# Optimization experiments

Measured on AMD Instinct MI355X. Metric: run time of the kernel, lower is better.

## Reference

```python
import jax, jax.numpy as jnp
import numpy as np

B, T, D = 16, 512, 512
T_OUT = 2560  # static cap on expanded length (mean total ~2048, +3 sigma << 2560)
MAX_DUR = 8.0


def setup_inputs() -> dict:
    key = jax.random.key(0)
    kx, kd = jax.random.split(key)
    x = jax.random.normal(kx, (B, T, D), dtype=jnp.float32)
    dur = jax.random.uniform(kd, (B, T), dtype=jnp.float32) * MAX_DUR
    return {"x": x, "dur": dur}


def reference(x, dur):
    # Rounded integer durations: (dur + 0.5).long() in torch == floor(dur + 0.5)
    d = jnp.floor(dur + 0.5).astype(jnp.int32)          # [B, T]
    ends = jnp.cumsum(d, axis=1)                         # [B, T] exclusive-end offsets
    pos = jnp.arange(T_OUT, dtype=jnp.int32)             # [T_OUT]
    # For output frame j, source phoneme = first t with ends[t] > j
    src = jax.vmap(lambda e: jnp.searchsorted(e, pos, side='right'))(ends)  # [B, T_OUT]
    src = jnp.minimum(src, x.shape[1] - 1)
    out = jnp.take_along_axis(x, src[:, :, None], axis=1)  # [B, T_OUT, D]
    valid = (pos[None, :] < ends[:, -1:]).astype(x.dtype)  # zero-pad beyond total length
    return out * valid[:, :, None]
```

## Files before the change

kernel.cpp:

```cpp
#include <hip/hip_runtime.h>
#include <math.h>


#define LR_B 16
#define LR_T 512
#define LR_D 512
#define LR_TOUT 2560

__global__ void lr_scan_kernel(const float* __restrict__ dur, int* __restrict__ ends) {
    const int b = blockIdx.x;
    const int t = threadIdx.x;
    __shared__ int s[LR_T];
    float dv = dur[b * LR_T + t];
    s[t] = (int)floorf(dv + 0.5f);
    __syncthreads();
    #pragma unroll
    for (int off = 1; off < LR_T; off <<= 1) {
        int v = (t >= off) ? s[t - off] : 0;
        __syncthreads();
        s[t] += v;
        __syncthreads();
    }
    ends[b * LR_T + t] = s[t];
}

__global__ void lr_expand_kernel(const float* __restrict__ x,
                                 const int* __restrict__ ends,
                                 float* __restrict__ out) {
    const int j = blockIdx.x;
    const int b = blockIdx.y;
    const int tid = threadIdx.x;

    const int* e = ends + b * LR_T;
    const int total = e[LR_T - 1];

    float4 val = make_float4(0.f, 0.f, 0.f, 0.f);
    if (j < total) {
        int lo = 0, hi = LR_T;
        while (lo < hi) {
            int mid = (lo + hi) >> 1;
            if (e[mid] > j) hi = mid; else lo = mid + 1;
        }
        int src = (lo < LR_T - 1) ? lo : (LR_T - 1);
        const float4* row = (const float4*)(x + (size_t)(b * LR_T + src) * LR_D);
        val = row[tid];
    }
    float4* orow = (float4*)(out + (size_t)(b * LR_TOUT + j) * LR_D);
    orow[tid] = val;
}

extern "C" void kernel_launch(void* const* d_in, const int* in_sizes, int n_in,
                              void* d_out, int out_size, void* d_ws, size_t ws_size,
                              hipStream_t stream) {
    const float* x   = (const float*)d_in[0];
    const float* dur = (const float*)d_in[1];
    float* out = (float*)d_out;
    int* ends = (int*)d_ws;

    lr_scan_kernel<<<LR_B, LR_T, 0, stream>>>(dur, ends);

    dim3 grid(LR_TOUT, LR_B);
    lr_expand_kernel<<<grid, 128, 0, stream>>>(x, ends, out);
}
```

Baseline: 112.4 us.

## Precompute source indices in scan kernel and process two rows per block

```diff
diff --git a/kernel.cpp b/kernel.cpp
--- a/kernel.cpp
+++ b/kernel.cpp
@@ -7,7 +7,7 @@
 #define LR_D 512
 #define LR_TOUT 2560
 
-__global__ void lr_scan_kernel(const float* __restrict__ dur, int* __restrict__ ends) {
+__global__ void lr_prep_kernel(const float* __restrict__ dur, int* __restrict__ src) {
     const int b = blockIdx.x;
     const int t = threadIdx.x;
     __shared__ int s[LR_T];
@@ -21,32 +21,43 @@
         s[t] += v;
         __syncthreads();
     }
-    ends[b * LR_T + t] = s[t];
+    const int total = s[LR_T - 1];
+    #pragma unroll
+    for (int k = 0; k < LR_TOUT / LR_T; ++k) {
+        const int j = t + k * LR_T;
+        int v;
+        if (j < total) {
+            int lo = 0, hi = LR_T;
+            #pragma unroll
+            for (int it = 0; it < 10; ++it) {
+                if (lo < hi) {
+                    int mid = (lo + hi) >> 1;
+                    if (s[mid] > j) hi = mid; else lo = mid + 1;
+                }
+            }
+            v = (lo < LR_T - 1) ? lo : (LR_T - 1);
+        } else {
+            v = -1;
+        }
+        src[b * LR_TOUT + j] = v;
+    }
 }
 
 __global__ void lr_expand_kernel(const float* __restrict__ x,
-                                 const int* __restrict__ ends,
+                                 const int* __restrict__ src,
                                  float* __restrict__ out) {
-    const int j = blockIdx.x;
     const int b = blockIdx.y;
-    const int tid = threadIdx.x;
+    const int j = blockIdx.x * 2 + (threadIdx.x >> 7);
+    const int lane = threadIdx.x & 127;
 
-    const int* e = ends + b * LR_T;
-    const int total = e[LR_T - 1];
-
+    const int si = src[b * LR_TOUT + j];
     float4 val = make_float4(0.f, 0.f, 0.f, 0.f);
-    if (j < total) {
-        int lo = 0, hi = LR_T;
-        while (lo < hi) {
-            int mid = (lo + hi) >> 1;
-            if (e[mid] > j) hi = mid; else lo = mid + 1;
-        }
-        int src = (lo < LR_T - 1) ? lo : (LR_T - 1);
-        const float4* row = (const float4*)(x + (size_t)(b * LR_T + src) * LR_D);
-        val = row[tid];
+    if (si >= 0) {
+        const float4* row = (const float4*)(x + (size_t)(b * LR_T + si) * LR_D);
+        val = row[lane];
     }
     float4* orow = (float4*)(out + (size_t)(b * LR_TOUT + j) * LR_D);
-    orow[tid] = val;
+    orow[lane] = val;
 }
 
 extern "C" void kernel_launch(void* const* d_in, const int* in_sizes, int n_in,
@@ -55,10 +66,10 @@
     const float* x   = (const float*)d_in[0];
     const float* dur = (const float*)d_in[1];
     float* out = (float*)d_out;
-    int* ends = (int*)d_ws;
+    int* src = (int*)d_ws;
 
-    lr_scan_kernel<<<LR_B, LR_T, 0, stream>>>(dur, ends);
+    lr_prep_kernel<<<LR_B, LR_T, 0, stream>>>(dur, src);
 
-    dim3 grid(LR_TOUT, LR_B);
-    lr_expand_kernel<<<grid, 128, 0, stream>>>(x, ends, out);
+    dim3 grid(LR_TOUT / 2, LR_B);
+    lr_expand_kernel<<<grid, 256, 0, stream>>>(x, src, out);
 }
```

New measurement: 107.1 us. 1.05x faster.
